# Kernel tuning notes

Hardware: AMD Instinct MI355X
Metric: run time of the kernel (lower is better)

## Reference

```python
import jax, jax.numpy as jnp
import numpy as np

B, T, C, H = 16, 2048, 1024, 64

def setup_inputs() -> dict:
    key = jax.random.key(0)
    kx, kq, kk, kv = jax.random.split(key, 4)
    x = jax.random.normal(kx, (B, T, C), dtype=jnp.float32)
    Wq = jax.random.normal(kq, (C, H), dtype=jnp.float32) * (C ** -0.5)
    Wk = jax.random.normal(kk, (C, H), dtype=jnp.float32) * (C ** -0.5)
    Wv = jax.random.normal(kv, (C, H), dtype=jnp.float32) * (C ** -0.5)
    return {"x": x, "Wq": Wq, "Wk": Wk, "Wv": Wv}

def reference(x, Wq, Wk, Wv):
    # single causal self-attention head; dropout p=0.0 (identity)
    Tlen = x.shape[1]
    q = jnp.einsum('btc,ch->bth', x, Wq)  # [B,T,H]
    k = jnp.einsum('btc,ch->bth', x, Wk)
    v = jnp.einsum('btc,ch->bth', x, Wv)
    scale = q.shape[-1] ** -0.5
    scores = jnp.einsum('bth,bsh->bts', q, k) * scale  # [B,T,T]
    causal = jnp.tril(jnp.ones((Tlen, Tlen), dtype=bool))
    scores = jnp.where(causal, scores, -jnp.inf)
    weights = jax.nn.softmax(scores, axis=-1)
    out = jnp.einsum('bts,bsh->bth', weights, v)  # [B,T,H]
    return out
```

## Files before the change

kernel.cpp:

```cpp
#include <hip/hip_runtime.h>


typedef float  floatx4 __attribute__((ext_vector_type(4)));
typedef __bf16 bf16x8  __attribute__((ext_vector_type(8)));
typedef short  short8v __attribute__((ext_vector_type(8)));
typedef unsigned short ushort4v __attribute__((ext_vector_type(4)));

constexpr int Bn = 16;
constexpr int Tn = 2048;
constexpr int Cn = 1024;
constexpr int Hn = 64;
constexpr int BT = Bn * Tn;

__device__ __forceinline__ unsigned short f2b(float f) {
  unsigned int u = __builtin_bit_cast(unsigned int, f);
  u += 0x7fffu + ((u >> 16) & 1u);
  return (unsigned short)(u >> 16);
}

__global__ __launch_bounds__(256) void pack_w(const float* __restrict__ Wq,
                                              const float* __restrict__ Wk,
                                              const float* __restrict__ Wv,
                                              unsigned short* __restrict__ Wp) {
  int gid = blockIdx.x * 256 + threadIdx.x;
  int mat = gid >> 16;
  int rem = gid & 65535;
  int k   = rem >> 6;
  int col = rem & 63;
  const float* W = (mat == 0) ? Wq : (mat == 1) ? Wk : Wv;
  float v = W[rem];
  int kb = k >> 3, j = k & 7, ct = (mat << 2) | (col >> 4), c = col & 15;
  size_t idx = ((((size_t)ct * 128) + kb) * 16 + c) * 8 + j;
  Wp[idx] = f2b(v);
}

__global__ __launch_bounds__(256) void proj_kernel(
    const float* __restrict__ x, const unsigned short* __restrict__ Wp,
    unsigned short* __restrict__ Q, unsigned short* __restrict__ K,
    unsigned short* __restrict__ Vt) {
  __shared__ alignas(16) unsigned short Al[64][72];
  __shared__ alignas(16) unsigned short Bl[12 * 1024];

  const int tid  = threadIdx.x;
  const int wave = tid >> 6;
  const int lane = tid & 63;
  const int quad = lane >> 4;
  const int l16  = lane & 15;
  const int wr   = wave >> 1;
  const int wc   = wave & 1;
  const int rbase = blockIdx.x * 64;

  floatx4 acc[2][6];
#pragma unroll
  for (int a = 0; a < 2; ++a)
#pragma unroll
    for (int b = 0; b < 6; ++b) acc[a][b] = (floatx4){0.f, 0.f, 0.f, 0.f};

  const int arow = tid >> 2;
  const int acol = (tid & 3) * 16;
  const float* xp = x + (size_t)(rbase + arow) * Cn + acol;

  for (int k0 = 0; k0 < Cn; k0 += 64) {
    floatx4 f0 = *reinterpret_cast<const floatx4*>(xp + k0);
    floatx4 f1 = *reinterpret_cast<const floatx4*>(xp + k0 + 4);
    floatx4 f2 = *reinterpret_cast<const floatx4*>(xp + k0 + 8);
    floatx4 f3 = *reinterpret_cast<const floatx4*>(xp + k0 + 12);

    if (k0) __syncthreads();

#pragma unroll
    for (int i = 0; i < 3; ++i) {
      const int ct = wave * 3 + i;
#pragma unroll
      for (int h = 0; h < 2; ++h) {
        const unsigned short* g =
            Wp + ((size_t)(ct * 128 + (k0 >> 3) + h * 4 + quad) * 16 + l16) * 8;
        __builtin_amdgcn_global_load_lds(
            (const __attribute__((address_space(1))) void*)g,
            (__attribute__((address_space(3))) void*)&Bl[ct * 1024 + h * 512],
            16, 0, 0);
      }
    }

    short8v p0, p1;
    p0[0] = (short)f2b(f0[0]); p0[1] = (short)f2b(f0[1]);
    p0[2] = (short)f2b(f0[2]); p0[3] = (short)f2b(f0[3]);
    p0[4] = (short)f2b(f1[0]); p0[5] = (short)f2b(f1[1]);
    p0[6] = (short)f2b(f1[2]); p0[7] = (short)f2b(f1[3]);
    p1[0] = (short)f2b(f2[0]); p1[1] = (short)f2b(f2[1]);
    p1[2] = (short)f2b(f2[2]); p1[3] = (short)f2b(f2[3]);
    p1[4] = (short)f2b(f3[0]); p1[5] = (short)f2b(f3[1]);
    p1[6] = (short)f2b(f3[2]); p1[7] = (short)f2b(f3[3]);
    *reinterpret_cast<short8v*>(&Al[arow][acol])     = p0;
    *reinterpret_cast<short8v*>(&Al[arow][acol + 8]) = p1;

    __syncthreads();

#pragma unroll
    for (int kk = 0; kk < 2; ++kk) {
      bf16x8 a0 = *reinterpret_cast<const bf16x8*>(
          &Al[wr * 32 + l16][kk * 32 + quad * 8]);
      bf16x8 a1 = *reinterpret_cast<const bf16x8*>(
          &Al[wr * 32 + 16 + l16][kk * 32 + quad * 8]);
#pragma unroll
      for (int c6 = 0; c6 < 6; ++c6) {
        const int ct = wc * 6 + c6;
        bf16x8 bfr = *reinterpret_cast<const bf16x8*>(
            &Bl[ct * 1024 + (kk * 4 + quad) * 128 + l16 * 8]);
        acc[0][c6] = __builtin_amdgcn_mfma_f32_16x16x32_bf16(a0, bfr, acc[0][c6], 0, 0, 0);
        acc[1][c6] = __builtin_amdgcn_mfma_f32_16x16x32_bf16(a1, bfr, acc[1][c6], 0, 0, 0);
      }
    }
  }

#pragma unroll
  for (int rt = 0; rt < 2; ++rt) {
#pragma unroll
    for (int c6 = 0; c6 < 6; ++c6) {
      const int cbase  = wc * 96 + c6 * 16;
      const int rowloc = wr * 32 + rt * 16 + quad * 4;
      if (cbase < 64) {
#pragma unroll
        for (int r = 0; r < 4; ++r)
          Q[(size_t)(rbase + rowloc + r) * Hn + cbase + l16] =
              f2b(acc[rt][c6][r] * 0.125f);
      } else if (cbase < 128) {
#pragma unroll
        for (int r = 0; r < 4; ++r)
          K[(size_t)(rbase + rowloc + r) * Hn + cbase - 64 + l16] =
              f2b(acc[rt][c6][r]);
      } else {
        const int b  = rbase >> 11;
        const int t0 = (rbase & 2047) + rowloc;
        const int h  = cbase - 128 + l16;
        ushort4v v;
#pragma unroll
        for (int r = 0; r < 4; ++r) v[r] = f2b(acc[rt][c6][r]);
        *reinterpret_cast<ushort4v*>(&Vt[((size_t)b * Hn + h) * Tn + t0]) = v;
      }
    }
  }
}

__global__ __launch_bounds__(256) void flash_kernel(
    const unsigned short* __restrict__ Q, const unsigned short* __restrict__ K,
    const unsigned short* __restrict__ Vt, float* __restrict__ out) {
  __shared__ alignas(16) unsigned short P[4][16][72];
  __shared__ alignas(16) float Om[4][16][68];
  __shared__ float Ml[4][16][2];

  const int tid  = threadIdx.x;
  const int wave = tid >> 6;
  const int lane = tid & 63;
  const int quad = lane >> 4;
  const int l16  = lane & 15;

  const int b   = blockIdx.x & 15;
  const int p16 = 127 - (blockIdx.x >> 4);
  const int qbase = p16 * 16;
  const int n_tiles  = (p16 >> 2) + 1;
  const int lastTile = p16 >> 2;
  const size_t bbase  = (size_t)b * Tn * Hn;
  const size_t vtbase = (size_t)b * Hn * Tn;

  bf16x8 qf[2];
#pragma unroll
  for (int i = 0; i < 2; ++i)
    qf[i] = *reinterpret_cast<const bf16x8*>(
        &Q[bbase + (size_t)(qbase + l16) * Hn + i * 32 + quad * 8]);

  floatx4 O[4];
#pragma unroll
  for (int i = 0; i < 4; ++i) O[i] = (floatx4){0.f, 0.f, 0.f, 0.f};
  float m_r[4], l_r[4];
#pragma unroll
  for (int r = 0; r < 4; ++r) { m_r[r] = -INFINITY; l_r[r] = 0.f; }

  for (int kt = wave; kt < n_tiles; kt += 4) {
    const int kvbase = kt * 64;

    floatx4 S[4];
#pragma unroll
    for (int ct = 0; ct < 4; ++ct) {
      floatx4 s = (floatx4){0.f, 0.f, 0.f, 0.f};
#pragma unroll
      for (int kk = 0; kk < 2; ++kk) {
        bf16x8 bfr = *reinterpret_cast<const bf16x8*>(
            &K[bbase + (size_t)(kvbase + ct * 16 + l16) * Hn + kk * 32 + quad * 8]);
        s = __builtin_amdgcn_mfma_f32_16x16x32_bf16(qf[kk], bfr, s, 0, 0, 0);
      }
      S[ct] = s;
    }

    bf16x8 vf[4][2];
#pragma unroll
    for (int ht = 0; ht < 4; ++ht)
#pragma unroll
      for (int kk = 0; kk < 2; ++kk)
        vf[ht][kk] = *reinterpret_cast<const bf16x8*>(
            &Vt[vtbase + (size_t)(ht * 16 + l16) * Tn + kvbase + kk * 32 + quad * 8]);

    if (kt == lastTile) {
#pragma unroll
      for (int ct = 0; ct < 4; ++ct)
#pragma unroll
        for (int r = 0; r < 4; ++r) {
          int trow = qbase + quad * 4 + r;
          int scol = kvbase + ct * 16 + l16;
          if (scol > trow) S[ct][r] = -1e30f;
        }
    }

#pragma unroll
    for (int r = 0; r < 4; ++r) {
      float mx = fmaxf(fmaxf(S[0][r], S[1][r]), fmaxf(S[2][r], S[3][r]));
#pragma unroll
      for (int d = 1; d < 16; d <<= 1) mx = fmaxf(mx, __shfl_xor(mx, d));
      float mnew  = fmaxf(m_r[r], mx);
      float alpha = __expf(m_r[r] - mnew);
      float rs = 0.f;
#pragma unroll
      for (int ct = 0; ct < 4; ++ct) {
        float p = __expf(S[ct][r] - mnew);
        S[ct][r] = p;
        rs += p;
      }
#pragma unroll
      for (int d = 1; d < 16; d <<= 1) rs += __shfl_xor(rs, d);
      l_r[r] = l_r[r] * alpha + rs;
      m_r[r] = mnew;
#pragma unroll
      for (int ct = 0; ct < 4; ++ct) O[ct][r] *= alpha;
#pragma unroll
      for (int ct = 0; ct < 4; ++ct)
        P[wave][quad * 4 + r][ct * 16 + l16] = f2b(S[ct][r]);
    }

    bf16x8 pf0 = *reinterpret_cast<const bf16x8*>(&P[wave][l16][quad * 8]);
    bf16x8 pf1 = *reinterpret_cast<const bf16x8*>(&P[wave][l16][32 + quad * 8]);
#pragma unroll
    for (int ht = 0; ht < 4; ++ht) {
      O[ht] = __builtin_amdgcn_mfma_f32_16x16x32_bf16(pf0, vf[ht][0], O[ht], 0, 0, 0);
      O[ht] = __builtin_amdgcn_mfma_f32_16x16x32_bf16(pf1, vf[ht][1], O[ht], 0, 0, 0);
    }
  }

#pragma unroll
  for (int ht = 0; ht < 4; ++ht)
#pragma unroll
    for (int r = 0; r < 4; ++r)
      Om[wave][quad * 4 + r][ht * 16 + l16] = O[ht][r];
  if (l16 == 0) {
#pragma unroll
    for (int r = 0; r < 4; ++r) {
      Ml[wave][quad * 4 + r][0] = m_r[r];
      Ml[wave][quad * 4 + r][1] = l_r[r];
    }
  }
  __syncthreads();

  {
    const int row = tid >> 4;
    const int c4  = (tid & 15) * 4;
    float m0 = Ml[0][row][0], m1 = Ml[1][row][0];
    float m2 = Ml[2][row][0], m3 = Ml[3][row][0];
    float M = fmaxf(fmaxf(m0, m1), fmaxf(m2, m3));
    float e0 = __expf(m0 - M), e1 = __expf(m1 - M);
    float e2 = __expf(m2 - M), e3 = __expf(m3 - M);
    float L = Ml[0][row][1] * e0 + Ml[1][row][1] * e1 +
              Ml[2][row][1] * e2 + Ml[3][row][1] * e3;
    float invL = 1.0f / L;
    floatx4 o0 = *reinterpret_cast<const floatx4*>(&Om[0][row][c4]);
    floatx4 o1 = *reinterpret_cast<const floatx4*>(&Om[1][row][c4]);
    floatx4 o2 = *reinterpret_cast<const floatx4*>(&Om[2][row][c4]);
    floatx4 o3 = *reinterpret_cast<const floatx4*>(&Om[3][row][c4]);
    floatx4 res;
#pragma unroll
    for (int j = 0; j < 4; ++j)
      res[j] = (o0[j] * e0 + o1[j] * e1 + o2[j] * e2 + o3[j] * e3) * invL;
    *reinterpret_cast<floatx4*>(
        &out[bbase + (size_t)(qbase + row) * Hn + c4]) = res;
  }
}

extern "C" void kernel_launch(void* const* d_in, const int* in_sizes, int n_in,
                              void* d_out, int out_size, void* d_ws, size_t ws_size,
                              hipStream_t stream) {
  const float* x  = (const float*)d_in[0];
  const float* Wq = (const float*)d_in[1];
  const float* Wk = (const float*)d_in[2];
  const float* Wv = (const float*)d_in[3];
  float* out = (float*)d_out;

  char* ws = (char*)d_ws;
  unsigned short* Q  = (unsigned short*)(ws);
  unsigned short* Kb = (unsigned short*)(ws + ((size_t)4 << 20));
  unsigned short* Vt = (unsigned short*)(ws + ((size_t)8 << 20));
  unsigned short* Wp = (unsigned short*)(ws + ((size_t)12 << 20));

  pack_w<<<dim3(768), dim3(256), 0, stream>>>(Wq, Wk, Wv, Wp);
  proj_kernel<<<dim3(BT / 64), dim3(256), 0, stream>>>(x, Wp, Q, Kb, Vt);
  flash_kernel<<<dim3(16 * 128), dim3(256), 0, stream>>>(Q, Kb, Vt, out);
}
```

Baseline: 270.5 us.

## Transpose attention MFMAs, use exp2 softmax, drop LDS staging of x

The projection kernel now converts x rows straight into MFMA A-fragments in registers with packed bf16 converts, removing the LDS staging buffer and its round trip. The flash kernel swaps MFMA operand order so each lane owns one query row, which cuts the per-row shuffle reductions to two xor steps. It also folds log2(e) into the Q scale so the softmax can use exp2, and writes P through an XOR-swizzled unpadded LDS tile using packed converts. setprio hints are added around the MFMA bursts; the main risks are the bank-conflict behaviour of the new swizzle and the layout correctness of the transposed accumulators.

```diff
diff --git a/kernel.cpp b/kernel.cpp
--- a/kernel.cpp
+++ b/kernel.cpp
@@ -3,8 +3,9 @@
 
 typedef float  floatx4 __attribute__((ext_vector_type(4)));
 typedef __bf16 bf16x8  __attribute__((ext_vector_type(8)));
-typedef short  short8v __attribute__((ext_vector_type(8)));
 typedef unsigned short ushort4v __attribute__((ext_vector_type(4)));
+typedef unsigned int   uint2v   __attribute__((ext_vector_type(2)));
+typedef unsigned int   uint4v   __attribute__((ext_vector_type(4)));
 
 constexpr int Bn = 16;
 constexpr int Tn = 2048;
@@ -12,10 +13,18 @@
 constexpr int Hn = 64;
 constexpr int BT = Bn * Tn;
 
+constexpr float QSCALE = 0.125f * 1.44269504088896340736f;
+
 __device__ __forceinline__ unsigned short f2b(float f) {
   unsigned int u = __builtin_bit_cast(unsigned int, f);
   u += 0x7fffu + ((u >> 16) & 1u);
   return (unsigned short)(u >> 16);
+}
+
+__device__ __forceinline__ unsigned int cvt_pk_bf16(float lo, float hi) {
+  unsigned int r;
+  asm("v_cvt_pk_bf16_f32 %0, %1, %2" : "=v"(r) : "v"(lo), "v"(hi));
+  return r;
 }
 
 __global__ __launch_bounds__(256) void pack_w(const float* __restrict__ Wq,
@@ -38,7 +47,6 @@
     const float* __restrict__ x, const unsigned short* __restrict__ Wp,
     unsigned short* __restrict__ Q, unsigned short* __restrict__ K,
     unsigned short* __restrict__ Vt) {
-  __shared__ alignas(16) unsigned short Al[64][72];
   __shared__ alignas(16) unsigned short Bl[12 * 1024];
 
   const int tid  = threadIdx.x;
@@ -56,15 +64,18 @@
 #pragma unroll
     for (int b = 0; b < 6; ++b) acc[a][b] = (floatx4){0.f, 0.f, 0.f, 0.f};
 
-  const int arow = tid >> 2;
-  const int acol = (tid & 3) * 16;
-  const float* xp = x + (size_t)(rbase + arow) * Cn + acol;
+  const float* xp = x + (size_t)(rbase + wr * 32 + l16) * Cn + quad * 8;
 
   for (int k0 = 0; k0 < Cn; k0 += 64) {
-    floatx4 f0 = *reinterpret_cast<const floatx4*>(xp + k0);
-    floatx4 f1 = *reinterpret_cast<const floatx4*>(xp + k0 + 4);
-    floatx4 f2 = *reinterpret_cast<const floatx4*>(xp + k0 + 8);
-    floatx4 f3 = *reinterpret_cast<const floatx4*>(xp + k0 + 12);
+    floatx4 fa[2][2][2];
+#pragma unroll
+    for (int rg = 0; rg < 2; ++rg) {
+      const float* bp = xp + rg * 16 * Cn + k0;
+      fa[rg][0][0] = *reinterpret_cast<const floatx4*>(bp);
+      fa[rg][0][1] = *reinterpret_cast<const floatx4*>(bp + 4);
+      fa[rg][1][0] = *reinterpret_cast<const floatx4*>(bp + 32);
+      fa[rg][1][1] = *reinterpret_cast<const floatx4*>(bp + 36);
+    }
 
     if (k0) __syncthreads();
 
@@ -82,33 +93,30 @@
       }
     }
 
-    short8v p0, p1;
-    p0[0] = (short)f2b(f0[0]); p0[1] = (short)f2b(f0[1]);
-    p0[2] = (short)f2b(f0[2]); p0[3] = (short)f2b(f0[3]);
-    p0[4] = (short)f2b(f1[0]); p0[5] = (short)f2b(f1[1]);
-    p0[6] = (short)f2b(f1[2]); p0[7] = (short)f2b(f1[3]);
-    p1[0] = (short)f2b(f2[0]); p1[1] = (short)f2b(f2[1]);
-    p1[2] = (short)f2b(f2[2]); p1[3] = (short)f2b(f2[3]);
-    p1[4] = (short)f2b(f3[0]); p1[5] = (short)f2b(f3[1]);
-    p1[6] = (short)f2b(f3[2]); p1[7] = (short)f2b(f3[3]);
-    *reinterpret_cast<short8v*>(&Al[arow][acol])     = p0;
-    *reinterpret_cast<short8v*>(&Al[arow][acol + 8]) = p1;
+    bf16x8 af[2][2];
+#pragma unroll
+    for (int rg = 0; rg < 2; ++rg)
+#pragma unroll
+      for (int kk = 0; kk < 2; ++kk) {
+        uint4v u;
+        u[0] = cvt_pk_bf16(fa[rg][kk][0][0], fa[rg][kk][0][1]);
+        u[1] = cvt_pk_bf16(fa[rg][kk][0][2], fa[rg][kk][0][3]);
+        u[2] = cvt_pk_bf16(fa[rg][kk][1][0], fa[rg][kk][1][1]);
+        u[3] = cvt_pk_bf16(fa[rg][kk][1][2], fa[rg][kk][1][3]);
+        af[rg][kk] = __builtin_bit_cast(bf16x8, u);
+      }
 
     __syncthreads();
 
 #pragma unroll
     for (int kk = 0; kk < 2; ++kk) {
-      bf16x8 a0 = *reinterpret_cast<const bf16x8*>(
-          &Al[wr * 32 + l16][kk * 32 + quad * 8]);
-      bf16x8 a1 = *reinterpret_cast<const bf16x8*>(
-          &Al[wr * 32 + 16 + l16][kk * 32 + quad * 8]);
 #pragma unroll
       for (int c6 = 0; c6 < 6; ++c6) {
         const int ct = wc * 6 + c6;
         bf16x8 bfr = *reinterpret_cast<const bf16x8*>(
             &Bl[ct * 1024 + (kk * 4 + quad) * 128 + l16 * 8]);
-        acc[0][c6] = __builtin_amdgcn_mfma_f32_16x16x32_bf16(a0, bfr, acc[0][c6], 0, 0, 0);
-        acc[1][c6] = __builtin_amdgcn_mfma_f32_16x16x32_bf16(a1, bfr, acc[1][c6], 0, 0, 0);
+        acc[0][c6] = __builtin_amdgcn_mfma_f32_16x16x32_bf16(af[0][kk], bfr, acc[0][c6], 0, 0, 0);
+        acc[1][c6] = __builtin_amdgcn_mfma_f32_16x16x32_bf16(af[1][kk], bfr, acc[1][c6], 0, 0, 0);
       }
     }
   }
@@ -123,7 +131,7 @@
 #pragma unroll
         for (int r = 0; r < 4; ++r)
           Q[(size_t)(rbase + rowloc + r) * Hn + cbase + l16] =
-              f2b(acc[rt][c6][r] * 0.125f);
+              f2b(acc[rt][c6][r] * QSCALE);
       } else if (cbase < 128) {
 #pragma unroll
         for (int r = 0; r < 4; ++r)
@@ -145,7 +153,7 @@
 __global__ __launch_bounds__(256) void flash_kernel(
     const unsigned short* __restrict__ Q, const unsigned short* __restrict__ K,
     const unsigned short* __restrict__ Vt, float* __restrict__ out) {
-  __shared__ alignas(16) unsigned short P[4][16][72];
+  __shared__ alignas(16) unsigned short P[4][16][64];
   __shared__ alignas(16) float Om[4][16][68];
   __shared__ float Ml[4][16][2];
 
@@ -172,25 +180,28 @@
   floatx4 O[4];
 #pragma unroll
   for (int i = 0; i < 4; ++i) O[i] = (floatx4){0.f, 0.f, 0.f, 0.f};
-  float m_r[4], l_r[4];
-#pragma unroll
-  for (int r = 0; r < 4; ++r) { m_r[r] = -INFINITY; l_r[r] = 0.f; }
+  float m_r = -INFINITY, l_r = 0.f;
+
+  const int swz  = (l16 & 7) << 3;
+  const int trow = qbase + l16;
 
   for (int kt = wave; kt < n_tiles; kt += 4) {
     const int kvbase = kt * 64;
 
     floatx4 S[4];
+    __builtin_amdgcn_s_setprio(1);
 #pragma unroll
     for (int ct = 0; ct < 4; ++ct) {
       floatx4 s = (floatx4){0.f, 0.f, 0.f, 0.f};
 #pragma unroll
       for (int kk = 0; kk < 2; ++kk) {
-        bf16x8 bfr = *reinterpret_cast<const bf16x8*>(
+        bf16x8 kf = *reinterpret_cast<const bf16x8*>(
             &K[bbase + (size_t)(kvbase + ct * 16 + l16) * Hn + kk * 32 + quad * 8]);
-        s = __builtin_amdgcn_mfma_f32_16x16x32_bf16(qf[kk], bfr, s, 0, 0, 0);
+        s = __builtin_amdgcn_mfma_f32_16x16x32_bf16(kf, qf[kk], s, 0, 0, 0);
       }
       S[ct] = s;
     }
+    __builtin_amdgcn_s_setprio(0);
 
     bf16x8 vf[4][2];
 #pragma unroll
@@ -204,58 +215,64 @@
 #pragma unroll
       for (int ct = 0; ct < 4; ++ct)
 #pragma unroll
-        for (int r = 0; r < 4; ++r) {
-          int trow = qbase + quad * 4 + r;
-          int scol = kvbase + ct * 16 + l16;
-          if (scol > trow) S[ct][r] = -1e30f;
-        }
-    }
-
-#pragma unroll
-    for (int r = 0; r < 4; ++r) {
-      float mx = fmaxf(fmaxf(S[0][r], S[1][r]), fmaxf(S[2][r], S[3][r]));
-#pragma unroll
-      for (int d = 1; d < 16; d <<= 1) mx = fmaxf(mx, __shfl_xor(mx, d));
-      float mnew  = fmaxf(m_r[r], mx);
-      float alpha = __expf(m_r[r] - mnew);
-      float rs = 0.f;
-#pragma unroll
-      for (int ct = 0; ct < 4; ++ct) {
-        float p = __expf(S[ct][r] - mnew);
+        for (int r = 0; r < 4; ++r)
+          if (kvbase + ct * 16 + quad * 4 + r > trow) S[ct][r] = -1e30f;
+    }
+
+    float mx0 = fmaxf(fmaxf(S[0][0], S[0][1]), fmaxf(S[0][2], S[0][3]));
+    float mx1 = fmaxf(fmaxf(S[1][0], S[1][1]), fmaxf(S[1][2], S[1][3]));
+    float mx2 = fmaxf(fmaxf(S[2][0], S[2][1]), fmaxf(S[2][2], S[2][3]));
+    float mx3 = fmaxf(fmaxf(S[3][0], S[3][1]), fmaxf(S[3][2], S[3][3]));
+    float mx  = fmaxf(fmaxf(mx0, mx1), fmaxf(mx2, mx3));
+    mx = fmaxf(mx, __shfl_xor(mx, 16));
+    mx = fmaxf(mx, __shfl_xor(mx, 32));
+    float mnew  = fmaxf(m_r, mx);
+    float alpha = __builtin_amdgcn_exp2f(m_r - mnew);
+    float rs = 0.f;
+#pragma unroll
+    for (int ct = 0; ct < 4; ++ct)
+#pragma unroll
+      for (int r = 0; r < 4; ++r) {
+        float p = __builtin_amdgcn_exp2f(S[ct][r] - mnew);
         S[ct][r] = p;
         rs += p;
       }
-#pragma unroll
-      for (int d = 1; d < 16; d <<= 1) rs += __shfl_xor(rs, d);
-      l_r[r] = l_r[r] * alpha + rs;
-      m_r[r] = mnew;
-#pragma unroll
-      for (int ct = 0; ct < 4; ++ct) O[ct][r] *= alpha;
-#pragma unroll
-      for (int ct = 0; ct < 4; ++ct)
-        P[wave][quad * 4 + r][ct * 16 + l16] = f2b(S[ct][r]);
-    }
-
-    bf16x8 pf0 = *reinterpret_cast<const bf16x8*>(&P[wave][l16][quad * 8]);
-    bf16x8 pf1 = *reinterpret_cast<const bf16x8*>(&P[wave][l16][32 + quad * 8]);
+    rs += __shfl_xor(rs, 16);
+    rs += __shfl_xor(rs, 32);
+    l_r = l_r * alpha + rs;
+    m_r = mnew;
+#pragma unroll
+    for (int ht = 0; ht < 4; ++ht)
+#pragma unroll
+      for (int r = 0; r < 4; ++r) O[ht][r] *= alpha;
+
+#pragma unroll
+    for (int ct = 0; ct < 4; ++ct) {
+      uint2v w;
+      w[0] = cvt_pk_bf16(S[ct][0], S[ct][1]);
+      w[1] = cvt_pk_bf16(S[ct][2], S[ct][3]);
+      *reinterpret_cast<uint2v*>(&P[wave][l16][(ct * 16 + quad * 4) ^ swz]) = w;
+    }
+    bf16x8 pf0 = *reinterpret_cast<const bf16x8*>(&P[wave][l16][(quad * 8) ^ swz]);
+    bf16x8 pf1 = *reinterpret_cast<const bf16x8*>(&P[wave][l16][(32 + quad * 8) ^ swz]);
+
+    __builtin_amdgcn_s_setprio(1);
 #pragma unroll
     for (int ht = 0; ht < 4; ++ht) {
-      O[ht] = __builtin_amdgcn_mfma_f32_16x16x32_bf16(pf0, vf[ht][0], O[ht], 0, 0, 0);
-      O[ht] = __builtin_amdgcn_mfma_f32_16x16x32_bf16(pf1, vf[ht][1], O[ht], 0, 0, 0);
-    }
+      O[ht] = __builtin_amdgcn_mfma_f32_16x16x32_bf16(vf[ht][0], pf0, O[ht], 0, 0, 0);
+      O[ht] = __builtin_amdgcn_mfma_f32_16x16x32_bf16(vf[ht][1], pf1, O[ht], 0, 0, 0);
+    }
+    __builtin_amdgcn_s_setprio(0);
   }
 
 #pragma unroll
   for (int ht = 0; ht < 4; ++ht)
 #pragma unroll
     for (int r = 0; r < 4; ++r)
-      Om[wave][quad * 4 + r][ht * 16 + l16] = O[ht][r];
-  if (l16 == 0) {
-#pragma unroll
-    for (int r = 0; r < 4; ++r) {
-      Ml[wave][quad * 4 + r][0] = m_r[r];
-      Ml[wave][quad * 4 + r][1] = l_r[r];
-    }
+      Om[wave][l16][ht * 16 + quad * 4 + r] = O[ht][r];
+  if (quad == 0) {
+    Ml[wave][l16][0] = m_r;
+    Ml[wave][l16][1] = l_r;
   }
   __syncthreads();
 
@@ -265,8 +282,8 @@
     float m0 = Ml[0][row][0], m1 = Ml[1][row][0];
     float m2 = Ml[2][row][0], m3 = Ml[3][row][0];
     float M = fmaxf(fmaxf(m0, m1), fmaxf(m2, m3));
-    float e0 = __expf(m0 - M), e1 = __expf(m1 - M);
-    float e2 = __expf(m2 - M), e3 = __expf(m3 - M);
+    float e0 = __builtin_amdgcn_exp2f(m0 - M), e1 = __builtin_amdgcn_exp2f(m1 - M);
+    float e2 = __builtin_amdgcn_exp2f(m2 - M), e3 = __builtin_amdgcn_exp2f(m3 - M);
     float L = Ml[0][row][1] * e0 + Ml[1][row][1] * e1 +
               Ml[2][row][1] * e2 + Ml[3][row][1] * e3;
     float invL = 1.0f / L;
```

Measured after the change: 275.6 us. About the same (+1.9%).
